# Kernel optimization log

Hardware: AMD Instinct MI355X
Metric: run time of the kernel (lower is better)

The kernel has to match this reference:

```python
import jax, jax.numpy as jnp
import numpy as np

# ---- DMP constants (DMPParameters(N=5, tau=1, dt=1/(T*l), Dof=1)) ----
N = 5
T = 10
L_SUB = 10
DT = 1.0 / (T * L_SUB)          # 0.01
A_X = 1.0
A_Z = 25.0
B_Z = A_Z / 4.0
TIME_STEPS = T * L_SUB + 1       # 101
_C = jnp.exp(-A_X * jnp.linspace(0.0, 1.0, N)).astype(jnp.float32)        # RBF centers
_SIGMA2 = ((N ** 1.5) / _C / A_X).astype(jnp.float32)                     # RBF widths


def _conv1d(x, w, b, pad):
    # x: [B, Cin, L], w: [Cout, Cin, K]
    y = jax.lax.conv_general_dilated(x, w, window_strides=(1,), padding=[(pad, pad)],
                                     dimension_numbers=("NCH", "OIH", "NCH"))
    return y + b[None, :, None]


def _forward(input, y0, conv1_w, conv1_b, conv2_w, conv2_b, fc_w, fc_b, L_w, L_b):
    B = input.shape[0]
    # ---- TSFEEGNet (CNN feature extractor) -> [B, 404] ----
    h = jax.nn.relu(_conv1d(input, conv1_w, conv1_b, 3))     # [B, 64, 384]
    h = h.reshape(B, h.shape[1], -1, 4).mean(-1)             # avgpool4 -> [B, 64, 96]
    h = jax.nn.relu(_conv1d(h, conv2_w, conv2_b, 2))         # [B, 128, 96]
    h = h.reshape(B, h.shape[1], -1, 4).mean(-1)             # [B, 128, 24]
    feat = h.reshape(B, -1)                                  # [B, 3072]
    output = feat @ fc_w.T + fc_b                            # [B, 404]
    # ---- s = L(output): per-sample time scaling tau ----
    s = output @ L_w.T + L_b                                 # [B, 1]
    tau = s[:, 0]                                            # [B]
    # ---- DMPIntegrator.forward (Dof=1): goal=output[:,0], w=output[:,1:6] ----
    goal = output[:, 0]                                      # [B]
    w = output[:, 1:1 + N]                                   # [B, N]
    y0v = y0.reshape(-1)                                     # [B]
    dy0 = jnp.zeros_like(y0v) + 0.01

    def step(carry, _):
        x, y, z = carry
        x = x + (-A_X * x * tau * DT)                        # canonical system
        psi = jnp.exp(-0.5 * (x[:, None] - _C[None, :]) ** 2 / _SIGMA2[None, :])  # [B, N]
        fx = (w * psi).sum(-1) * x * (goal - y0v) / psi.sum(-1)
        dz = A_Z * (B_Z * (goal - y) - z) + fx
        dy = z
        y = y + dy * tau * DT
        z = z + dz * tau * DT
        return (x, y, z), y

    x0 = jnp.ones_like(y0v)
    z0 = dy0 * tau
    _, Ys = jax.lax.scan(step, (x0, y0v, z0), None, length=TIME_STEPS - 1)  # [T-1, B]
    Y = jnp.concatenate([y0v[None, :], Ys], axis=0)          # [T, B]
    y_traj = Y.T.reshape(B, 1, TIME_STEPS)                   # [B, Dof=1, T]
    return y_traj.transpose(0, 2, 1)                         # [B, T, 1]


def setup_inputs():
    key = jax.random.key(0)
    ks = jax.random.split(key, 10)
    B = 4096
    sc = 0.05
    return {
        "input": jax.random.normal(ks[0], (B, 5, 384), jnp.float32),
        "y0": jax.random.normal(ks[1], (B,), jnp.float32),
        "conv1_w": jax.random.normal(ks[2], (64, 5, 7), jnp.float32) * sc,
        "conv1_b": jax.random.normal(ks[3], (64,), jnp.float32) * sc,
        "conv2_w": jax.random.normal(ks[4], (128, 64, 5), jnp.float32) * sc,
        "conv2_b": jax.random.normal(ks[5], (128,), jnp.float32) * sc,
        "fc_w": jax.random.normal(ks[6], (404, 3072), jnp.float32) * sc,
        "fc_b": jax.random.normal(ks[7], (404,), jnp.float32) * sc,
        "L_w": jax.random.normal(ks[8], (1, 404), jnp.float32) * sc,
        "L_b": jax.random.normal(ks[9], (1,), jnp.float32) * sc,
    }


def reference(input, y0, conv1_w, conv1_b, conv2_w, conv2_b, fc_w, fc_b, L_w, L_b):
    return _forward(input, y0, conv1_w, conv1_b, conv2_w, conv2_b, fc_w, fc_b, L_w, L_b)
```

## Files before the change

kernel.cpp:

```cpp
#include <hip/hip_runtime.h>
#include <math.h>


typedef _Float16 f16x8 __attribute__((ext_vector_type(8)));
typedef float f32x4  __attribute__((ext_vector_type(4)));
typedef float f32x16 __attribute__((ext_vector_type(16)));
typedef int   i32x4  __attribute__((ext_vector_type(4)));

union Frag { int u[4]; i32x4 q; f16x8 h; };
union H16 { _Float16 hf; unsigned short us; };

__device__ __forceinline__ unsigned short f16_rne(float f) {
    H16 c; c.hf = (_Float16)f; return c.us;
}

#define ZERO16 {0.f,0.f,0.f,0.f,0.f,0.f,0.f,0.f,0.f,0.f,0.f,0.f,0.f,0.f,0.f,0.f}

__global__ void precompute_kernel(const float* __restrict__ w1,
                                  const float* __restrict__ w2,
                                  const float* __restrict__ fc_w,
                                  const float* __restrict__ fc_b,
                                  const float* __restrict__ L_w,
                                  const float* __restrict__ L_b,
                                  float* __restrict__ fc7,
                                  float* __restrict__ taub,
                                  unsigned* __restrict__ wfrag1,
                                  unsigned* __restrict__ wfrag2) {
    const int t = threadIdx.x, bb = blockIdx.x;
    if (bb < 48) {
        __shared__ float part[7][64];
        const int k = bb * 64 + (t & 63), jc = t >> 6;
        const int j0 = jc * 51;
        float s = 0.f;
        #pragma unroll 8
        for (int j = j0; j < j0 + 51 && j < 404; ++j)
            s += L_w[j] * fc_w[j * 3072 + k];
        if (jc) part[jc - 1][t & 63] = s;
        __syncthreads();
        if (jc == 0) {
            const int kk = t & 63;
            const int oc = k / 24, fq = k - oc * 24;
            float r[8];
            #pragma unroll
            for (int j = 0; j < 6; ++j) r[j] = fc_w[j * 3072 + k];
            float tv = s;
            #pragma unroll
            for (int j = 0; j < 7; ++j) tv += part[j][kk];
            r[6] = tv; r[7] = 0.f;
            #pragma unroll
            for (int j = 0; j < 8; ++j) fc7[fq * 1024 + j * 128 + oc] = r[j];
        }
    } else if (bb == 48) {
        if (t < 64) {
            float s = 0.f;
            for (int j = t; j < 404; j += 64) s += L_w[j] * fc_b[j];
            #pragma unroll
            for (int off = 32; off; off >>= 1) s += __shfl_down(s, off);
            if (t == 0) taub[0] = s + L_b[0];
        }
        if (t < 384) {
            const int lane = t & 63, nt = (t >> 6) & 1, ks = t >> 7;
            const int oc = nt * 32 + (lane & 31);
            unsigned short h[8];
            #pragma unroll
            for (int j = 0; j < 8; ++j) {
                const int kp = ks * 16 + (lane >> 5) * 8 + j;
                const int ic = kp >> 3, dk = kp & 7;
                const float v = (ic < 5 && dk < 7)
                              ? w1[oc * 35 + ic * 7 + dk] * 1024.0f : 0.f;
                h[j] = f16_rne(v);
            }
            #pragma unroll
            for (int wj = 0; wj < 4; ++wj)
                wfrag1[t * 4 + wj] = ((unsigned)h[2 * wj + 1] << 16) | h[2 * wj];
        }
    } else {
        const int i = (bb - 49) * 512 + t;
        const int lane = i & 63, nt = (i >> 6) & 3, step = i >> 8;
        const int oc = nt * 32 + (lane & 31);
        const int dk = step >> 2, icc = step & 3;
        unsigned short h[8];
        #pragma unroll
        for (int j = 0; j < 8; ++j) {
            const int ic = icc * 16 + (lane >> 5) * 8 + j;
            const float v = w2[oc * 320 + ic * 5 + dk] * 1024.0f;
            h[j] = f16_rne(v);
        }
        #pragma unroll
        for (int wj = 0; wj < 4; ++wj)
            wfrag2[i * 4 + wj] = ((unsigned)h[2 * wj + 1] << 16) | h[2 * wj];
    }
}

__global__ __launch_bounds__(256, 5) void fused_kernel(
    const float* __restrict__ input,
    const float* __restrict__ b1,
    const float* __restrict__ b2,
    const unsigned* __restrict__ wfrag1,
    const unsigned* __restrict__ wfrag2,
    const float* __restrict__ fc7,
    const float* __restrict__ fc_b,
    const float* __restrict__ taubp,
    float* __restrict__ params)
{
    __shared__ unsigned lds_in[1960];
    __shared__ __align__(16) unsigned short h1f[7200];
    __shared__ float red[32];

    const int t = threadIdx.x, b = blockIdx.x;
    const int lane = t & 63, w = t >> 6;
    const int lq = lane & 31, hi = lane >> 5;

    if (t < 40) {
        const int r = t >> 3, c = t & 7;
        lds_in[r * 392 + ((c < 3) ? c : 384 + c)] = 0u;
    }
    if (t >= 64 && t < 208) {
        const int i = t - 64;
        const int r = i / 36, wd = i - r * 36;
        const int row = (r < 2) ? r : 96 + r;
        ((unsigned*)h1f)[row * 36 + wd] = 0u;
    }
    const float4* inb4 = (const float4*)(input + (size_t)b * 1920);
    for (int i = t; i < 480; i += 256) {
        const float4 v = inb4[i];
        const int x4 = i * 4, ic = x4 / 384, x = x4 - ic * 384;
        unsigned* dst = lds_in + ic * 392 + 3 + x;
        dst[0] = (unsigned)f16_rne(v.x);
        dst[1] = (unsigned)f16_rne(v.y);
        dst[2] = (unsigned)f16_rne(v.z);
        dst[3] = (unsigned)f16_rne(v.w);
    }
    __syncthreads();

    const i32x4* w1f = (const i32x4*)wfrag1;
    Frag c1b[3][2];
    #pragma unroll
    for (int ks = 0; ks < 3; ++ks)
        #pragma unroll
        for (int nt = 0; nt < 2; ++nt)
            c1b[ks][nt].q = w1f[(ks * 2 + nt) * 64 + lane];
    float b1v[2];
    #pragma unroll
    for (int nt = 0; nt < 2; ++nt) b1v[nt] = b1[nt * 32 + lq];

    unsigned pbuf[2][8];
    {
        const unsigned* src = lds_in + hi * 392 + (w * 3) * 32 + lq;
        #pragma unroll
        for (int j = 0; j < 8; ++j) pbuf[0][j] = src[j];
    }
    #pragma unroll
    for (int m = 0; m < 3; ++m) {
        const int mtile = w * 3 + m;
        f32x16 acc0 = ZERO16, acc1 = ZERO16;
        #pragma unroll
        for (int ks = 0; ks < 3; ++ks) {
            const int it = m * 3 + ks, cur = it & 1, nxt = cur ^ 1;
            if (it < 8) {
                const int nit = it + 1, nm = nit / 3, nks = nit % 3;
                const int rowoff = (nks == 2) ? 4 * 392 : (nks * 2 + hi) * 392;
                const unsigned* src = lds_in + rowoff + (w * 3 + nm) * 32 + lq;
                #pragma unroll
                for (int j = 0; j < 8; ++j) pbuf[nxt][j] = src[j];
            }
            Frag af;
            #pragma unroll
            for (int wj = 0; wj < 4; ++wj)
                af.u[wj] = __builtin_amdgcn_perm(pbuf[cur][2*wj+1], pbuf[cur][2*wj], 0x05040100u);
            if (ks == 2) {
                #pragma unroll
                for (int wj = 0; wj < 4; ++wj) af.u[wj] = hi ? 0 : af.u[wj];
            }
            __builtin_amdgcn_s_setprio(1);
            acc0 = __builtin_amdgcn_mfma_f32_32x32x16_f16(af.h, c1b[ks][0].h, acc0, 0, 0, 0);
            acc1 = __builtin_amdgcn_mfma_f32_32x32x16_f16(af.h, c1b[ks][1].h, acc1, 0, 0, 0);
            __builtin_amdgcn_s_setprio(0);
        }
        #pragma unroll
        for (int q = 0; q < 4; ++q) {
            const int c = mtile * 8 + 2 * q + hi;
            {
                float s = 0.f;
                #pragma unroll
                for (int r4 = 0; r4 < 4; ++r4)
                    s += fmaxf(acc0[q*4+r4] * 0.0009765625f + b1v[0], 0.f);
                h1f[(c + 2) * 72 + lq] = f16_rne(0.25f * s);
            }
            {
                float s = 0.f;
                #pragma unroll
                for (int r4 = 0; r4 < 4; ++r4)
                    s += fmaxf(acc1[q*4+r4] * 0.0009765625f + b1v[1], 0.f);
                h1f[(c + 2) * 72 + 32 + lq] = f16_rne(0.25f * s);
            }
        }
    }
    __syncthreads();

    f32x16 acc2[3] = {ZERO16, ZERO16, ZERO16};

    const i32x4* aF = (const i32x4*)(h1f + lq * 72 + hi * 8);
    const i32x4* w2f = (const i32x4*)wfrag2;
    Frag b2b[3];
    Frag a2f[2][3];

    {
        b2b[0].q = w2f[w * 64 + lane];
        b2b[1].q = w2f[(4 + w) * 64 + lane];
        #pragma unroll
        for (int mt = 0; mt < 3; ++mt) a2f[0][mt].q = aF[mt * 288];
    }

    #pragma unroll
    for (int s = 0; s < 20; ++s) {
        const int sb = s % 3, ab = s & 1, an = ab ^ 1;
        if (s < 18)
            b2b[(s + 2) % 3].q = w2f[((s + 2) * 4 + w) * 64 + lane];
        if (s < 19) {
            const int dkn = (s + 1) >> 2, iccn = (s + 1) & 3;
            #pragma unroll
            for (int mt = 0; mt < 3; ++mt)
                a2f[an][mt].q = aF[(mt * 32 + dkn) * 9 + iccn * 2];
        }
        __builtin_amdgcn_s_setprio(1);
        #pragma unroll
        for (int mt = 0; mt < 3; ++mt)
            acc2[mt] = __builtin_amdgcn_mfma_f32_32x32x16_f16(a2f[ab][mt].h, b2b[sb].h, acc2[mt], 0, 0, 0);
        __builtin_amdgcn_s_setprio(0);
    }

    float dot[7] = {0.f, 0.f, 0.f, 0.f, 0.f, 0.f, 0.f};
    {
        const float b2v = b2[w * 32 + lq];
        #pragma unroll
        for (int mt = 0; mt < 3; ++mt) {
            #pragma unroll
            for (int q = 0; q < 4; ++q) {
                float s = 0.f;
                #pragma unroll
                for (int r4 = 0; r4 < 4; ++r4)
                    s += fmaxf(acc2[mt][q*4+r4] * 0.0009765625f + b2v, 0.f);
                s *= 0.25f;
                const int fq = mt * 8 + 2 * q + hi;
                const float* fp = fc7 + fq * 1024 + w * 32 + lq;
                float f[7];
                #pragma unroll
                for (int j = 0; j < 7; ++j) f[j] = fp[j * 128];
                #pragma unroll
                for (int j = 0; j < 7; ++j) dot[j] += s * f[j];
            }
        }
    }

    #pragma unroll
    for (int j = 0; j < 7; ++j) {
        float s = dot[j];
        #pragma unroll
        for (int off = 32; off; off >>= 1) s += __shfl_down(s, off);
        if (lane == 0) red[w * 8 + j] = s;
    }
    __syncthreads();
    if (t < 7) {
        float s = red[t] + red[8 + t] + red[16 + t] + red[24 + t];
        s += (t < 6) ? fc_b[t] : taubp[0];
        params[(size_t)b * 8 + t] = s;
    }
}

__global__ void rollout_kernel(const float* __restrict__ params,
                               const float* __restrict__ y0,
                               float* __restrict__ out) {
    const int b = blockIdx.x * 256 + threadIdx.x;
    const float* p = params + (size_t)b * 8;
    const float goal = p[0];
    const float w0 = p[1], w1 = p[2], w2 = p[3], w3 = p[4], w4 = p[5];
    const float tau = p[6];
    const float y0v = y0[b];

    const float c0 = 1.0f;
    const float c1 = 0.77880078307140486825f;
    const float c2 = 0.60653065971263342360f;
    const float c3 = 0.47236655274101470714f;
    const float c4 = 0.36787944117144232160f;
    const float inv2s = -0.5f / 11.180339887498949f;
    const float e0 = inv2s * c0, e1 = inv2s * c1, e2 = inv2s * c2,
                e3 = inv2s * c3, e4 = inv2s * c4;

    float x = 1.0f, y = y0v, z = 0.01f * tau;
    const float td = tau * 0.01f;
    const float gmy0 = goal - y0v;
    float* ob = out + (size_t)b * 101;
    ob[0] = y0v;
    for (int s = 1; s <= 100; ++s) {
        x = x - x * td;
        const float d0 = x - c0, d1 = x - c1, d2 = x - c2, d3 = x - c3, d4 = x - c4;
        const float p0 = __expf(e0 * d0 * d0);
        const float p1 = __expf(e1 * d1 * d1);
        const float p2 = __expf(e2 * d2 * d2);
        const float p3 = __expf(e3 * d3 * d3);
        const float p4 = __expf(e4 * d4 * d4);
        const float den = p0 + p1 + p2 + p3 + p4;
        const float num = w0 * p0 + w1 * p1 + w2 * p2 + w3 * p3 + w4 * p4;
        const float fx = (num / den) * x * gmy0;
        const float dz = 25.0f * (6.25f * (goal - y) - z) + fx;
        const float dy = z;
        y += dy * td;
        z += dz * td;
        ob[s] = y;
    }
}

extern "C" void kernel_launch(void* const* d_in, const int* in_sizes, int n_in,
                              void* d_out, int out_size, void* d_ws, size_t ws_size,
                              hipStream_t stream) {
    const float* input = (const float*)d_in[0];
    const float* y0    = (const float*)d_in[1];
    const float* w1    = (const float*)d_in[2];
    const float* b1    = (const float*)d_in[3];
    const float* w2    = (const float*)d_in[4];
    const float* b2    = (const float*)d_in[5];
    const float* fc_w  = (const float*)d_in[6];
    const float* fc_b  = (const float*)d_in[7];
    const float* L_w   = (const float*)d_in[8];
    const float* L_b   = (const float*)d_in[9];
    float* out = (float*)d_out;

    float* ws      = (float*)d_ws;
    float* fc7     = ws;
    float* taub    = ws + 24576;
    float* params  = ws + 24640;
    unsigned* wfrag1 = (unsigned*)(ws + 57408);
    unsigned* wfrag2 = wfrag1 + 4096;

    const int B = in_sizes[1];

    precompute_kernel<<<59, 512, 0, stream>>>(w1, w2, fc_w, fc_b, L_w, L_b,
                                              fc7, taub, wfrag1, wfrag2);
    fused_kernel<<<B, 256, 0, stream>>>(input, b1, b2, wfrag1, wfrag2,
                                        fc7, fc_b, taub, params);
    rollout_kernel<<<B / 256, 256, 0, stream>>>(params, y0, out);
}
```

Before: 85.12 us.

## Fuse DMP rollout into fused kernel tail and widen precompute grid

The separate rollout kernel is removed, and each block of the fused CNN kernel now runs the 100-step DMP integration for its own sample on thread 0 after the final reduction. This drops one kernel launch and the params round trip through global memory. The precompute kernel's L_w·fc_w reduction is also split across 96 blocks of 32 columns instead of 48 blocks of 64, for more parallelism. The trade-off is a long serial tail on a single thread per block, which holds block resources and may lower throughput, and scalar strided stores of the output.

```diff
diff --git a/kernel.cpp b/kernel.cpp
--- a/kernel.cpp
+++ b/kernel.cpp
@@ -27,30 +27,30 @@
                                   unsigned* __restrict__ wfrag1,
                                   unsigned* __restrict__ wfrag2) {
     const int t = threadIdx.x, bb = blockIdx.x;
-    if (bb < 48) {
-        __shared__ float part[7][64];
-        const int k = bb * 64 + (t & 63), jc = t >> 6;
-        const int j0 = jc * 51;
+    if (bb < 96) {
+        __shared__ float part[15][32];
+        const int k = bb * 32 + (t & 31), jc = t >> 5;
+        const int j0 = jc * 26;
         float s = 0.f;
         #pragma unroll 8
-        for (int j = j0; j < j0 + 51 && j < 404; ++j)
+        for (int j = j0; j < j0 + 26 && j < 404; ++j)
             s += L_w[j] * fc_w[j * 3072 + k];
-        if (jc) part[jc - 1][t & 63] = s;
+        if (jc) part[jc - 1][t & 31] = s;
         __syncthreads();
         if (jc == 0) {
-            const int kk = t & 63;
+            const int kk = t & 31;
             const int oc = k / 24, fq = k - oc * 24;
             float r[8];
             #pragma unroll
             for (int j = 0; j < 6; ++j) r[j] = fc_w[j * 3072 + k];
             float tv = s;
             #pragma unroll
-            for (int j = 0; j < 7; ++j) tv += part[j][kk];
+            for (int j = 0; j < 15; ++j) tv += part[j][kk];
             r[6] = tv; r[7] = 0.f;
             #pragma unroll
             for (int j = 0; j < 8; ++j) fc7[fq * 1024 + j * 128 + oc] = r[j];
         }
-    } else if (bb == 48) {
+    } else if (bb == 96) {
         if (t < 64) {
             float s = 0.f;
             for (int j = t; j < 404; j += 64) s += L_w[j] * fc_b[j];
@@ -75,7 +75,7 @@
                 wfrag1[t * 4 + wj] = ((unsigned)h[2 * wj + 1] << 16) | h[2 * wj];
         }
     } else {
-        const int i = (bb - 49) * 512 + t;
+        const int i = (bb - 97) * 512 + t;
         const int lane = i & 63, nt = (i >> 6) & 3, step = i >> 8;
         const int oc = nt * 32 + (lane & 31);
         const int dk = step >> 2, icc = step & 3;
@@ -101,7 +101,8 @@
     const float* __restrict__ fc7,
     const float* __restrict__ fc_b,
     const float* __restrict__ taubp,
-    float* __restrict__ params)
+    const float* __restrict__ y0,
+    float* __restrict__ out)
 {
     __shared__ unsigned lds_in[1960];
     __shared__ __align__(16) unsigned short h1f[7200];
@@ -261,53 +262,53 @@
         if (lane == 0) red[w * 8 + j] = s;
     }
     __syncthreads();
-    if (t < 7) {
-        float s = red[t] + red[8 + t] + red[16 + t] + red[24 + t];
-        s += (t < 6) ? fc_b[t] : taubp[0];
-        params[(size_t)b * 8 + t] = s;
-    }
-}
-
-__global__ void rollout_kernel(const float* __restrict__ params,
-                               const float* __restrict__ y0,
-                               float* __restrict__ out) {
-    const int b = blockIdx.x * 256 + threadIdx.x;
-    const float* p = params + (size_t)b * 8;
-    const float goal = p[0];
-    const float w0 = p[1], w1 = p[2], w2 = p[3], w3 = p[4], w4 = p[5];
-    const float tau = p[6];
-    const float y0v = y0[b];
-
-    const float c0 = 1.0f;
-    const float c1 = 0.77880078307140486825f;
-    const float c2 = 0.60653065971263342360f;
-    const float c3 = 0.47236655274101470714f;
-    const float c4 = 0.36787944117144232160f;
-    const float inv2s = -0.5f / 11.180339887498949f;
-    const float e0 = inv2s * c0, e1 = inv2s * c1, e2 = inv2s * c2,
-                e3 = inv2s * c3, e4 = inv2s * c4;
-
-    float x = 1.0f, y = y0v, z = 0.01f * tau;
-    const float td = tau * 0.01f;
-    const float gmy0 = goal - y0v;
-    float* ob = out + (size_t)b * 101;
-    ob[0] = y0v;
-    for (int s = 1; s <= 100; ++s) {
-        x = x - x * td;
-        const float d0 = x - c0, d1 = x - c1, d2 = x - c2, d3 = x - c3, d4 = x - c4;
-        const float p0 = __expf(e0 * d0 * d0);
-        const float p1 = __expf(e1 * d1 * d1);
-        const float p2 = __expf(e2 * d2 * d2);
-        const float p3 = __expf(e3 * d3 * d3);
-        const float p4 = __expf(e4 * d4 * d4);
-        const float den = p0 + p1 + p2 + p3 + p4;
-        const float num = w0 * p0 + w1 * p1 + w2 * p2 + w3 * p3 + w4 * p4;
-        const float fx = (num / den) * x * gmy0;
-        const float dz = 25.0f * (6.25f * (goal - y) - z) + fx;
-        const float dy = z;
-        y += dy * td;
-        z += dz * td;
-        ob[s] = y;
+
+    if (t == 0) {
+        float pv[7];
+        #pragma unroll
+        for (int j = 0; j < 7; ++j)
+            pv[j] = red[j] + red[8 + j] + red[16 + j] + red[24 + j];
+        const float goal = pv[0] + fc_b[0];
+        const float w0p = pv[1] + fc_b[1];
+        const float w1p = pv[2] + fc_b[2];
+        const float w2p = pv[3] + fc_b[3];
+        const float w3p = pv[4] + fc_b[4];
+        const float w4p = pv[5] + fc_b[5];
+        const float tau = pv[6] + taubp[0];
+        const float y0v = y0[b];
+
+        const float c0 = 1.0f;
+        const float c1 = 0.77880078307140486825f;
+        const float c2 = 0.60653065971263342360f;
+        const float c3 = 0.47236655274101470714f;
+        const float c4 = 0.36787944117144232160f;
+        const float inv2s = -0.5f / 11.180339887498949f;
+        const float e0 = inv2s * c0, e1 = inv2s * c1, e2 = inv2s * c2,
+                    e3 = inv2s * c3, e4 = inv2s * c4;
+
+        float x = 1.0f, y = y0v, z = 0.01f * tau;
+        const float td = tau * 0.01f;
+        const float gmy0 = goal - y0v;
+        float* ob = out + (size_t)b * 101;
+        ob[0] = y0v;
+        for (int s = 1; s <= 100; ++s) {
+            x = x - x * td;
+            const float d0 = x - c0, d1 = x - c1, d2 = x - c2,
+                        d3 = x - c3, d4 = x - c4;
+            const float p0 = __expf(e0 * d0 * d0);
+            const float p1 = __expf(e1 * d1 * d1);
+            const float p2 = __expf(e2 * d2 * d2);
+            const float p3 = __expf(e3 * d3 * d3);
+            const float p4 = __expf(e4 * d4 * d4);
+            const float den = p0 + p1 + p2 + p3 + p4;
+            const float num = w0p * p0 + w1p * p1 + w2p * p2 + w3p * p3 + w4p * p4;
+            const float fx = (num / den) * x * gmy0;
+            const float dz = 25.0f * (6.25f * (goal - y) - z) + fx;
+            const float dy = z;
+            y += dy * td;
+            z += dz * td;
+            ob[s] = y;
+        }
     }
 }
 
@@ -329,15 +330,13 @@
     float* ws      = (float*)d_ws;
     float* fc7     = ws;
     float* taub    = ws + 24576;
-    float* params  = ws + 24640;
-    unsigned* wfrag1 = (unsigned*)(ws + 57408);
+    unsigned* wfrag1 = (unsigned*)(ws + 24640);
     unsigned* wfrag2 = wfrag1 + 4096;
 
     const int B = in_sizes[1];
 
-    precompute_kernel<<<59, 512, 0, stream>>>(w1, w2, fc_w, fc_b, L_w, L_b,
-                                              fc7, taub, wfrag1, wfrag2);
+    precompute_kernel<<<107, 512, 0, stream>>>(w1, w2, fc_w, fc_b, L_w, L_b,
+                                               fc7, taub, wfrag1, wfrag2);
     fused_kernel<<<B, 256, 0, stream>>>(input, b1, b2, wfrag1, wfrag2,
-                                        fc7, fc_b, taub, params);
-    rollout_kernel<<<B / 256, 256, 0, stream>>>(params, y0, out);
+                                        fc7, fc_b, taub, y0, out);
 }
```

Result: slower. 112.0 us (+31.6%).
